# Performance work log

Measured on AMD Instinct MI355X. Metric: run time of the kernel, lower is better.

## Reference

```python
import jax, jax.numpy as jnp
import numpy as np
from jax import lax

EPS = 1e-5
DN = ('NCHW', 'OIHW', 'NCHW')

def _quant_global(w):
    scale = 1.0 / jnp.maximum(jnp.mean(jnp.abs(w)), EPS)
    u = jnp.clip(jnp.round(w * scale), -1.0, 1.0)
    return u, scale

def _quant_per_channel_dw(w):
    # w: [O, 1, kH, kW]; mean |w| over the kernel taps per output channel
    m = jnp.mean(jnp.abs(w).reshape(w.shape[0], w.shape[1], -1), axis=2, keepdims=True)
    scale = 1.0 / jnp.maximum(m, EPS)[..., None]          # [O,1,1,1]
    u = jnp.clip(jnp.round(w * scale), -1.0, 1.0)
    scale_bcast = jnp.transpose(scale, (1, 0, 2, 3))      # [1,O,1,1] broadcasts over y's channels
    return u, scale_bcast

def _ste(w_real, u):
    # straight-through estimator: forward uses u, grad flows to w_real
    return w_real + lax.stop_gradient(u - w_real)

def setup_inputs() -> dict:
    key = jax.random.key(0)
    k1, k2, k3 = jax.random.split(key, 3)
    x = jax.random.normal(k1, (16, 384, 56, 56), dtype=jnp.float32)
    w_dw = jax.random.normal(k2, (384, 1, 3, 3), dtype=jnp.float32) * 0.1
    w_pw = jax.random.normal(k3, (384, 384, 1, 1), dtype=jnp.float32) * 0.05
    return {"x": x, "w_dw": w_dw, "w_pw": w_pw}

def reference(x, w_dw, w_pw):
    C = x.shape[1]
    # depthwise HardTernaryConv (groups=in_chn, per-channel quant, pad=k//2)
    u_dw, s_dw = _quant_per_channel_dw(w_dw)
    y = lax.conv_general_dilated(x, _ste(w_dw, u_dw), window_strides=(1, 1),
                                 padding=((1, 1), (1, 1)),
                                 dimension_numbers=DN, feature_group_count=C)
    y = y / s_dw
    # pointwise 1x1 HardTernaryConv (global scalar quant scale)
    u_pw, s_pw = _quant_global(w_pw)
    y = lax.conv_general_dilated(y, _ste(w_pw, u_pw), window_strides=(1, 1),
                                 padding=((0, 0), (0, 0)), dimension_numbers=DN)
    y = y / s_pw
    return y
```

## Files before the change

### kernel.cpp

```cpp
#include <hip/hip_runtime.h>
#include <hip/hip_bf16.h>

#define CH 384
#define HH 56
#define WW 56
#define HW (HH*WW)
#define NN 16
#define BN 112
#define BK 64

#define XR_STRIDE 3840
#define YS_PITCH 18

typedef __attribute__((ext_vector_type(4))) float f32x4;
typedef __attribute__((ext_vector_type(8))) short bf16x8;
typedef __attribute__((ext_vector_type(4))) unsigned int u32x4;

__device__ float          g_wdw_eff[CH * 9];
__device__ __hip_bfloat16 g_wpw_u[CH * CH];
__device__ float          g_mx_pw;

__global__ __launch_bounds__(256) void partial_kernel(const float* __restrict__ wpw,
                                                      double* __restrict__ part) {
    const int t = threadIdx.x;
    const int base = blockIdx.x * 1536;
    double s = 0.0;
    #pragma unroll
    for (int k = 0; k < 6; ++k) s += (double)fabsf(wpw[base + t + k * 256]);
    #pragma unroll
    for (int off = 32; off > 0; off >>= 1) s += __shfl_down(s, off, 64);
    __shared__ double sred[4];
    if ((t & 63) == 0) sred[t >> 6] = s;
    __syncthreads();
    if (t == 0) part[blockIdx.x] = ((sred[0] + sred[1]) + sred[2]) + sred[3];
}

__global__ __launch_bounds__(512) void quant_kernel(const float* __restrict__ wdw,
                                                    const float* __restrict__ wpw,
                                                    const double* __restrict__ part) {
    const int t = threadIdx.x;
    __shared__ double pl[96];
    __shared__ float s_scale, s_mx;
    if (t < 96) pl[t] = part[t];
    __syncthreads();
    if (t == 0) {
        double tot = 0.0;
        #pragma unroll
        for (int i = 0; i < 96; ++i) tot += pl[i];
        const float mean = (float)(tot / (double)(CH * CH));
        const float mx   = fmaxf(mean, 1e-5f);
        s_mx = mx;
        s_scale = 1.0f / mx;
    }
    __syncthreads();
    const float scale = s_scale;

    const int base = blockIdx.x * 4096 + t * 8;
    const float4 a = *reinterpret_cast<const float4*>(wpw + base);
    const float4 b = *reinterpret_cast<const float4*>(wpw + base + 4);
    const float vin[8] = {a.x, a.y, a.z, a.w, b.x, b.y, b.z, b.w};
    bf16x8 uo;
    #pragma unroll
    for (int k = 0; k < 8; ++k) {
        float u = rintf(vin[k] * scale);
        u = fminf(1.f, fmaxf(-1.f, u));
        __hip_bfloat16 h = __float2bfloat16(u);
        uo[k] = *reinterpret_cast<short*>(&h);
    }
    *reinterpret_cast<bf16x8*>(g_wpw_u + base) = uo;

    if (blockIdx.x == 0) {
        if (t == 0) g_mx_pw = s_mx;
        if (t < CH) {
            const float* w = wdw + t * 9;
            float asum = 0.f;
            #pragma unroll
            for (int k = 0; k < 9; ++k) asum += fabsf(w[k]);
            const float mxd = fmaxf(asum / 9.0f, 1e-5f);
            const float scd = 1.0f / mxd;
            #pragma unroll
            for (int k = 0; k < 9; ++k) {
                float u = rintf(w[k] * scd);
                u = fminf(1.f, fmaxf(-1.f, u));
                g_wdw_eff[t * 9 + k] = u * mxd;
            }
        }
    }
}

__global__ __launch_bounds__(448, 4) void dw_kernel(const float* __restrict__ x,
                                                    __hip_bfloat16* __restrict__ y) {
    __shared__ __attribute__((aligned(16))) char xs[12 * XR_STRIDE];
    __shared__ __attribute__((aligned(16))) __hip_bfloat16 ys[224 * YS_PITCH];

    const int bid  = blockIdx.x;
    const int orig = (bid & 7) * 96 + (bid >> 3);
    const int nc   = orig >> 1;
    const int half = orig & 1;
    const int n    = nc / 24;
    const int cig  = nc % 24;
    const int ci0  = cig * 16;

    const int t    = threadIdx.x;
    const int wv   = t >> 6;
    const int lane = t & 63;

    const int cil = t & 15;
    const int rw  = t >> 4;
    const int row = rw / 7;
    const int wc  = rw % 7;
    const int w0  = wc * 8;

    const float* xg = x + ((size_t)n * CH + ci0) * HW;

    float wt[9];
    {
        const float* wdp = g_wdw_eff + (ci0 + cil) * 9;
        #pragma unroll
        for (int k = 0; k < 9; ++k) wt[k] = wdp[k];
    }

    const int hbase = half * 28;

    #pragma unroll
    for (int kk = 0; kk < 4; ++kk) {
        const int q = wv + 7 * kk;
        if (q < 24) {
            const int ro  = q >> 2;
            const int sub = q & 3;
            const int R   = hbase - 1 + ro;
            const int rr  = (R + 12) % 12;
            const int Rc  = R < 0 ? 0 : (R > HH - 1 ? HH - 1 : R);
            const int s   = sub * 64 + lane;
            const int sci = s / 15;
            const int scl = s - sci * 15;
            if (s < 240 && scl < 14) {
                __builtin_amdgcn_global_load_lds(
                    (const __attribute__((address_space(1))) void*)
                        (xg + (size_t)sci * HW + Rc * WW + scl * 4),
                    (__attribute__((address_space(3))) void*)
                        (xs + rr * XR_STRIDE + sub * 1024),
                    16, 0, 0);
            }
        }
    }

    #pragma unroll
    for (int i = 0; i < 7; ++i) {
        const int h0 = hbase + i * 4;

        if (i < 6) {
            const int RB = h0 + 5;
            #pragma unroll
            for (int kk = 0; kk < 3; ++kk) {
                const int q = wv + 7 * kk;
                if (q < 16) {
                    const int ro  = q >> 2;
                    const int sub = q & 3;
                    const int R   = RB + ro;
                    const int rr  = R % 12;
                    const int Rc  = R > HH - 1 ? HH - 1 : R;
                    const int s   = sub * 64 + lane;
                    const int sci = s / 15;
                    const int scl = s - sci * 15;
                    if (s < 240 && scl < 14) {
                        __builtin_amdgcn_global_load_lds(
                            (const __attribute__((address_space(1))) void*)
                                (xg + (size_t)sci * HW + Rc * WW + scl * 4),
                            (__attribute__((address_space(3))) void*)
                                (xs + rr * XR_STRIDE + sub * 1024),
                            16, 0, 0);
                    }
                }
            }
            if (wv < 2) asm volatile("s_waitcnt vmcnt(3)" ::: "memory");
            else        asm volatile("s_waitcnt vmcnt(2)" ::: "memory");
        } else {
            asm volatile("s_waitcnt vmcnt(0)" ::: "memory");
        }
        __builtin_amdgcn_s_barrier();
        __builtin_amdgcn_sched_barrier(0);

        const int h   = h0 + row;
        const int rrb = (h0 + 11) % 12;

        float acc[8] = {0.f, 0.f, 0.f, 0.f, 0.f, 0.f, 0.f, 0.f};
        #pragma unroll
        for (int r = 0; r < 3; ++r) {
            int rr = rrb + row + r; if (rr >= 12) rr -= 12;
            const char* rowp = xs + rr * XR_STRIDE + (cil * 15 + 2 * wc) * 16;
            const f32x4 f0 = *reinterpret_cast<const f32x4*>(rowp);
            const f32x4 f1 = *reinterpret_cast<const f32x4*>(rowp + 16);
            const float e0 = (wc > 0) ? *reinterpret_cast<const float*>(rowp - 4) : 0.f;
            const float f8 = *reinterpret_cast<const float*>(rowp + 32);
            const float x9 = (wc < 6) ? f8 : 0.f;
            const float xv[10] = {e0, f0.x, f0.y, f0.z, f0.w,
                                  f1.x, f1.y, f1.z, f1.w, x9};
            const bool dead = (r == 0 && h == 0) || (r == 2 && h == HH - 1);
            #pragma unroll
            for (int d = 0; d < 3; ++d) {
                const float w3 = dead ? 0.f : wt[r * 3 + d];
                #pragma unroll
                for (int j = 0; j < 8; ++j) acc[j] += w3 * xv[j + d];
            }
        }

        const int pxb = row * WW + w0;
        #pragma unroll
        for (int j = 0; j < 8; ++j)
            ys[(pxb + j) * YS_PITCH + cil] = __float2bfloat16(acc[j]);

        asm volatile("s_waitcnt lgkmcnt(0)" ::: "memory");
        __builtin_amdgcn_s_barrier();
        __builtin_amdgcn_sched_barrier(0);

        {
            const int px  = t >> 1;
            const int oct = t & 1;
            const unsigned* yp =
                reinterpret_cast<const unsigned*>(ys + px * YS_PITCH + oct * 8);
            u32x4 v;
            v.x = yp[0]; v.y = yp[1]; v.z = yp[2]; v.w = yp[3];
            *reinterpret_cast<u32x4*>(
                y + ((size_t)n * HW + (size_t)h0 * WW + px) * CH + ci0 + oct * 8) = v;
        }
        __builtin_amdgcn_sched_barrier(0);
    }
}

#define STAGE(B, KC) do {                                                         \
    const int _k0 = (KC) * BK;                                                    \
    _Pragma("unroll")                                                             \
    for (int _i = 0; _i < 4; ++_i) {                                              \
        const int _sb = wv * 4 + _i;                                              \
        if (_sb < 14) {                                                           \
            const int _s  = _sb * 64 + lane;                                      \
            const int _p  = _s >> 3;                                              \
            const int _c8 = (_s & 7) ^ (_p & 7);                                  \
            __builtin_amdgcn_global_load_lds(                                     \
                (const __attribute__((address_space(1))) void*)                  \
                    (yb + (size_t)_p * CH + _k0 + _c8 * 8),                       \
                (__attribute__((address_space(3))) void*)                        \
                    (&blds[(B)][0] + _sb * 512),                                  \
                16, 0, 0);                                                        \
        }                                                                         \
    }                                                                             \
} while (0)

#define LOADA(dst, KC) {                                                          \
    dst[0][0] = *reinterpret_cast<const bf16x8*>(ap0 + (KC) * 64);                \
    dst[0][1] = *reinterpret_cast<const bf16x8*>(ap0 + (KC) * 64 + 32);           \
    dst[1][0] = *reinterpret_cast<const bf16x8*>(ap1 + (KC) * 64);                \
    dst[1][1] = *reinterpret_cast<const bf16x8*>(ap1 + (KC) * 64 + 32); }

__global__ __launch_bounds__(256) void pw_kernel(const __hip_bfloat16* __restrict__ y,
                                                 float* __restrict__ out) {
    __shared__ __attribute__((aligned(16))) __hip_bfloat16 blds[2][BN * BK];

    const int bid  = blockIdx.x;
    const int orig = (bid & 7) * 168 + (bid >> 3);
    const int n  = orig / 84;
    const int r  = orig % 84;
    const int pt = r / 3;
    const int cb = r % 3;
    const int wv   = threadIdx.x >> 6;
    const int lane = threadIdx.x & 63;
    const int lr   = lane & 15;
    const int lk   = lane >> 4;

    const __hip_bfloat16* yb = y + ((size_t)n * HW + (size_t)pt * BN) * CH;
    const __hip_bfloat16* ap0 = g_wpw_u + (size_t)(cb * 128 + wv * 32 + lr) * CH + 8 * lk;
    const __hip_bfloat16* ap1 = ap0 + (size_t)16 * CH;

    f32x4 acc[2][7];
    #pragma unroll
    for (int i = 0; i < 2; ++i)
        #pragma unroll
        for (int j = 0; j < 7; ++j) acc[i][j] = (f32x4){0.f, 0.f, 0.f, 0.f};

    bf16x8 areg[2][2][2];
    STAGE(0, 0);
    LOADA(areg[0], 0);
    __syncthreads();

    #pragma unroll
    for (int kc = 0; kc < 6; ++kc) {
        const int cur = kc & 1;
        if (kc < 5) { STAGE(cur ^ 1, kc + 1); LOADA(areg[cur ^ 1], kc + 1); }
        #pragma unroll
        for (int kk = 0; kk < 2; ++kk) {
            bf16x8 bfr[7];
            #pragma unroll
            for (int j = 0; j < 7; ++j) {
                const int p  = 16 * j + lr;
                const int c8 = (kk * 4 + lk) ^ (p & 7);
                bfr[j] = *reinterpret_cast<const bf16x8*>(&blds[cur][p * 64 + c8 * 8]);
            }
            #pragma unroll
            for (int i = 0; i < 2; ++i)
                #pragma unroll
                for (int j = 0; j < 7; ++j)
                    acc[i][j] = __builtin_amdgcn_mfma_f32_16x16x32_bf16(
                        areg[cur][i][kk], bfr[j], acc[i][j], 0, 0, 0);
        }
        __syncthreads();
    }

    const float s = g_mx_pw;
    float* ob = out + (size_t)n * CH * HW + (size_t)pt * BN;
    #pragma unroll
    for (int i = 0; i < 2; ++i) {
        const int co0 = cb * 128 + wv * 32 + i * 16 + lk * 4;
        #pragma unroll
        for (int j = 0; j < 7; ++j) {
            const int px = 16 * j + lr;
            #pragma unroll
            for (int rr = 0; rr < 4; ++rr)
                ob[(size_t)(co0 + rr) * HW + px] = acc[i][j][rr] * s;
        }
    }
}

__global__ __launch_bounds__(512) void fused_kernel(const float* __restrict__ x,
                                                    float* __restrict__ out) {
    __shared__ __attribute__((aligned(16))) __hip_bfloat16 ylds[64 * CH];
    const int bid  = blockIdx.x;
    const int orig = (bid & 7) * 112 + (bid >> 3);
    const int n = orig / HH, h = orig % HH;
    const float* xn = x + (size_t)n * CH * HW;

    for (int u = threadIdx.x; u < CH * 7; u += 512) {
        const int ci = u / 7;
        const int wc = u % 7;
        const int w0 = wc * 8;
        const float* xp = xn + (size_t)ci * HW;
        const float* wd = g_wdw_eff + ci * 9;
        float acc[8] = {0.f, 0.f, 0.f, 0.f, 0.f, 0.f, 0.f, 0.f};
        #pragma unroll
        for (int dy = -1; dy <= 1; ++dy) {
            const int hh = h + dy;
            if (hh < 0 || hh >= HH) continue;
            const float* row = xp + hh * WW;
            const float4 va = *reinterpret_cast<const float4*>(row + w0);
            const float4 vb = *reinterpret_cast<const float4*>(row + w0 + 4);
            const float left  = (w0 > 0)      ? row[w0 - 1] : 0.f;
            const float right = (w0 + 8 < WW) ? row[w0 + 8] : 0.f;
            const float xv[10] = {left, va.x, va.y, va.z, va.w,
                                  vb.x, vb.y, vb.z, vb.w, right};
            #pragma unroll
            for (int dx = 0; dx < 3; ++dx) {
                const float wvv = wd[(dy + 1) * 3 + dx];
                #pragma unroll
                for (int j = 0; j < 8; ++j) acc[j] += xv[j + dx] * wvv;
            }
        }
        #pragma unroll
        for (int j = 0; j < 8; ++j)
            ylds[(w0 + j) * CH + (ci ^ ((j ^ wc) << 3))] = __float2bfloat16(acc[j]);
    }
    __syncthreads();

    const int wv   = threadIdx.x >> 6;
    const int lane = threadIdx.x & 63;
    const int lr   = lane & 15;
    const int lk   = lane >> 4;
    f32x4 acc[3][4];
    #pragma unroll
    for (int i = 0; i < 3; ++i)
        #pragma unroll
        for (int j = 0; j < 4; ++j) acc[i][j] = (f32x4){0.f, 0.f, 0.f, 0.f};
    const __hip_bfloat16* abase = g_wpw_u + (size_t)(wv * 16 + lr) * CH + 8 * lk;
    for (int k0 = 0; k0 < CH; k0 += 32) {
        bf16x8 bfr[4];
        #pragma unroll
        for (int j = 0; j < 4; ++j) {
            const int row = 16 * j + lr;
            const int sw  = ((row & 7) ^ ((row >> 3) & 7)) << 3;
            bfr[j] = *reinterpret_cast<const bf16x8*>(&ylds[row * CH + ((k0 + 8 * lk) ^ sw)]);
        }
        #pragma unroll
        for (int i = 0; i < 3; ++i) {
            const bf16x8 afr = *reinterpret_cast<const bf16x8*>(abase + (size_t)(i * 128) * CH + k0);
            #pragma unroll
            for (int j = 0; j < 4; ++j)
                acc[i][j] = __builtin_amdgcn_mfma_f32_16x16x32_bf16(afr, bfr[j], acc[i][j], 0, 0, 0);
        }
    }
    const float s = g_mx_pw;
    float* obase = out + (size_t)n * CH * HW + (size_t)h * WW;
    #pragma unroll
    for (int j = 0; j < 4; ++j) {
        const int pix = 16 * j + lr;
        if (pix >= WW) continue;
        #pragma unroll
        for (int i = 0; i < 3; ++i) {
            const int co0 = (wv + 8 * i) * 16 + lk * 4;
            #pragma unroll
            for (int rr = 0; rr < 4; ++rr)
                obase[(size_t)(co0 + rr) * HW + pix] = acc[i][j][rr] * s;
        }
    }
}

extern "C" void kernel_launch(void* const* d_in, const int* in_sizes, int n_in,
                              void* d_out, int out_size, void* d_ws, size_t ws_size,
                              hipStream_t stream) {
    const float* x    = (const float*)d_in[0];
    const float* w_dw = (const float*)d_in[1];
    const float* w_pw = (const float*)d_in[2];
    float* out = (float*)d_out;

    const size_t y_bytes    = (size_t)NN * HW * CH * sizeof(__hip_bfloat16);
    const size_t part_bytes = 96 * sizeof(double);

    if (ws_size >= y_bytes + part_bytes) {
        double* part = (double*)((char*)d_ws + y_bytes);
        partial_kernel<<<96, 256, 0, stream>>>(w_pw, part);
        quant_kernel<<<36, 512, 0, stream>>>(w_dw, w_pw, part);
        __hip_bfloat16* yg = (__hip_bfloat16*)d_ws;
        dw_kernel<<<768, 448, 0, stream>>>(x, yg);
        pw_kernel<<<NN * 28 * 3, 256, 0, stream>>>(yg, out);
    } else if (ws_size >= part_bytes) {
        double* part = (double*)d_ws;
        partial_kernel<<<96, 256, 0, stream>>>(w_pw, part);
        quant_kernel<<<36, 512, 0, stream>>>(w_dw, w_pw, part);
        fused_kernel<<<NN * HH, 512, 0, stream>>>(x, out);
    }
}
```

Before: 65.02 us.

## Retile depthwise kernel to 32 channels by quarter-height with smaller LDS ring

The depthwise stage now has each block cover 32 channels over a 14-row quarter of the image, processing 2 rows per step, where it used to cover 16 channels over half the image at 4 rows per step. The LDS row ring drops from 12 to 6 rows and the transposed bf16 staging buffer shrinks, so occupancy is raised to 6 blocks per CU. Output stores write 64 contiguous bytes of channels per pixel instead of 32. In exchange, halo rows are reloaded more often relative to useful rows, and the waitcnt schedule is more intricate.

```diff
diff --git a/kernel.cpp b/kernel.cpp
--- a/kernel.cpp
+++ b/kernel.cpp
@@ -9,8 +9,9 @@
 #define BN 112
 #define BK 64
 
-#define XR_STRIDE 3840
-#define YS_PITCH 18
+#define XRING 6
+#define XRROW 7168
+#define YSP 34
 
 typedef __attribute__((ext_vector_type(4))) float f32x4;
 typedef __attribute__((ext_vector_type(8))) short bf16x8;
@@ -88,30 +89,41 @@
     }
 }
 
-__global__ __launch_bounds__(448, 4) void dw_kernel(const float* __restrict__ x,
+__global__ __launch_bounds__(448, 6) void dw_kernel(const float* __restrict__ x,
                                                     __hip_bfloat16* __restrict__ y) {
-    __shared__ __attribute__((aligned(16))) char xs[12 * XR_STRIDE];
-    __shared__ __attribute__((aligned(16))) __hip_bfloat16 ys[224 * YS_PITCH];
+    __shared__ __attribute__((aligned(16))) char xs[XRING * XRROW];
+    __shared__ __attribute__((aligned(16))) __hip_bfloat16 ys[112 * YSP];
 
     const int bid  = blockIdx.x;
     const int orig = (bid & 7) * 96 + (bid >> 3);
-    const int nc   = orig >> 1;
-    const int half = orig & 1;
-    const int n    = nc / 24;
-    const int cig  = nc % 24;
-    const int ci0  = cig * 16;
+    const int n    = orig / 48;
+    const int rem  = orig - n * 48;
+    const int cig  = rem >> 2;
+    const int qtr  = rem & 3;
+    const int ci0  = cig * 32;
+    const int qb   = qtr * 14;
 
     const int t    = threadIdx.x;
     const int wv   = t >> 6;
     const int lane = t & 63;
 
-    const int cil = t & 15;
-    const int rw  = t >> 4;
-    const int row = rw / 7;
-    const int wc  = rw % 7;
-    const int w0  = wc * 8;
-
-    const float* xg = x + ((size_t)n * CH + ci0) * HW;
+    const int slot = wv * 64 + lane;
+    const int sci  = slot / 14;
+    const int scl  = slot - sci * 14;
+    const float* xg    = x + ((size_t)n * CH + ci0) * HW;
+    const float* sbase = xg + (size_t)sci * HW + scl * 4;
+    char* sdst = xs + wv * 1024;
+
+    const int cil  = t / 14;
+    const int rm   = t - cil * 14;
+    const int rowp = rm / 7;
+    const int wc   = rm - rowp * 7;
+    const int w0   = wc * 8;
+
+    const int dpx = t >> 2;
+    const int dg  = t & 3;
+    const int drow = (dpx >= WW) ? 1 : 0;
+    const int dw_  = dpx - drow * WW;
 
     float wt[9];
     {
@@ -120,80 +132,48 @@
         for (int k = 0; k < 9; ++k) wt[k] = wdp[k];
     }
 
-    const int hbase = half * 28;
-
-    #pragma unroll
-    for (int kk = 0; kk < 4; ++kk) {
-        const int q = wv + 7 * kk;
-        if (q < 24) {
-            const int ro  = q >> 2;
-            const int sub = q & 3;
-            const int R   = hbase - 1 + ro;
-            const int rr  = (R + 12) % 12;
-            const int Rc  = R < 0 ? 0 : (R > HH - 1 ? HH - 1 : R);
-            const int s   = sub * 64 + lane;
-            const int sci = s / 15;
-            const int scl = s - sci * 15;
-            if (s < 240 && scl < 14) {
+    #pragma unroll
+    for (int k = 0; k < 4; ++k) {
+        int R = qb - 1 + k;
+        const int rr = (R + XRING) % XRING;
+        R = R < 0 ? 0 : R;
+        __builtin_amdgcn_global_load_lds(
+            (const __attribute__((address_space(1))) void*)(sbase + (size_t)R * WW),
+            (__attribute__((address_space(3))) void*)(sdst + rr * XRROW), 16, 0, 0);
+    }
+
+    #pragma unroll
+    for (int i = 0; i < 7; ++i) {
+        const int h0 = qb + 2 * i;
+        if (i < 6) {
+            #pragma unroll
+            for (int k = 0; k < 2; ++k) {
+                int R = h0 + 3 + k;
+                const int rr = R % XRING;
+                R = R > HH - 1 ? HH - 1 : R;
                 __builtin_amdgcn_global_load_lds(
-                    (const __attribute__((address_space(1))) void*)
-                        (xg + (size_t)sci * HW + Rc * WW + scl * 4),
-                    (__attribute__((address_space(3))) void*)
-                        (xs + rr * XR_STRIDE + sub * 1024),
-                    16, 0, 0);
+                    (const __attribute__((address_space(1))) void*)(sbase + (size_t)R * WW),
+                    (__attribute__((address_space(3))) void*)(sdst + rr * XRROW), 16, 0, 0);
             }
-        }
-    }
-
-    #pragma unroll
-    for (int i = 0; i < 7; ++i) {
-        const int h0 = hbase + i * 4;
-
-        if (i < 6) {
-            const int RB = h0 + 5;
-            #pragma unroll
-            for (int kk = 0; kk < 3; ++kk) {
-                const int q = wv + 7 * kk;
-                if (q < 16) {
-                    const int ro  = q >> 2;
-                    const int sub = q & 3;
-                    const int R   = RB + ro;
-                    const int rr  = R % 12;
-                    const int Rc  = R > HH - 1 ? HH - 1 : R;
-                    const int s   = sub * 64 + lane;
-                    const int sci = s / 15;
-                    const int scl = s - sci * 15;
-                    if (s < 240 && scl < 14) {
-                        __builtin_amdgcn_global_load_lds(
-                            (const __attribute__((address_space(1))) void*)
-                                (xg + (size_t)sci * HW + Rc * WW + scl * 4),
-                            (__attribute__((address_space(3))) void*)
-                                (xs + rr * XR_STRIDE + sub * 1024),
-                            16, 0, 0);
-                    }
-                }
-            }
-            if (wv < 2) asm volatile("s_waitcnt vmcnt(3)" ::: "memory");
-            else        asm volatile("s_waitcnt vmcnt(2)" ::: "memory");
+            if (i == 0) asm volatile("s_waitcnt vmcnt(2)" ::: "memory");
+            else        asm volatile("s_waitcnt vmcnt(3)" ::: "memory");
         } else {
-            asm volatile("s_waitcnt vmcnt(0)" ::: "memory");
+            asm volatile("s_waitcnt vmcnt(1)" ::: "memory");
         }
         __builtin_amdgcn_s_barrier();
         __builtin_amdgcn_sched_barrier(0);
 
-        const int h   = h0 + row;
-        const int rrb = (h0 + 11) % 12;
-
+        const int h = h0 + rowp;
         float acc[8] = {0.f, 0.f, 0.f, 0.f, 0.f, 0.f, 0.f, 0.f};
         #pragma unroll
         for (int r = 0; r < 3; ++r) {
-            int rr = rrb + row + r; if (rr >= 12) rr -= 12;
-            const char* rowp = xs + rr * XR_STRIDE + (cil * 15 + 2 * wc) * 16;
-            const f32x4 f0 = *reinterpret_cast<const f32x4*>(rowp);
-            const f32x4 f1 = *reinterpret_cast<const f32x4*>(rowp + 16);
-            const float e0 = (wc > 0) ? *reinterpret_cast<const float*>(rowp - 4) : 0.f;
-            const float f8 = *reinterpret_cast<const float*>(rowp + 32);
-            const float x9 = (wc < 6) ? f8 : 0.f;
+            const int rr = (h - 1 + r + XRING) % XRING;
+            const char* rp = xs + rr * XRROW + cil * 224 + wc * 32;
+            const f32x4 f0 = *reinterpret_cast<const f32x4*>(rp);
+            const f32x4 f1 = *reinterpret_cast<const f32x4*>(rp + 16);
+            float e0 = 0.f, x9 = 0.f;
+            if (wc > 0) e0 = *reinterpret_cast<const float*>(rp - 4);
+            if (wc < 6) x9 = *reinterpret_cast<const float*>(rp + 32);
             const float xv[10] = {e0, f0.x, f0.y, f0.z, f0.w,
                                   f1.x, f1.y, f1.z, f1.w, x9};
             const bool dead = (r == 0 && h == 0) || (r == 2 && h == HH - 1);
@@ -204,25 +184,22 @@
                 for (int j = 0; j < 8; ++j) acc[j] += w3 * xv[j + d];
             }
         }
-
-        const int pxb = row * WW + w0;
         #pragma unroll
         for (int j = 0; j < 8; ++j)
-            ys[(pxb + j) * YS_PITCH + cil] = __float2bfloat16(acc[j]);
+            ys[(rowp * WW + w0 + j) * YSP + cil] = __float2bfloat16(acc[j]);
 
         asm volatile("s_waitcnt lgkmcnt(0)" ::: "memory");
         __builtin_amdgcn_s_barrier();
         __builtin_amdgcn_sched_barrier(0);
 
         {
-            const int px  = t >> 1;
-            const int oct = t & 1;
             const unsigned* yp =
-                reinterpret_cast<const unsigned*>(ys + px * YS_PITCH + oct * 8);
+                reinterpret_cast<const unsigned*>(ys + dpx * YSP + dg * 8);
             u32x4 v;
             v.x = yp[0]; v.y = yp[1]; v.z = yp[2]; v.w = yp[3];
             *reinterpret_cast<u32x4*>(
-                y + ((size_t)n * HW + (size_t)h0 * WW + px) * CH + ci0 + oct * 8) = v;
+                y + ((size_t)n * HW + (size_t)(h0 + drow) * WW + dw_) * CH
+                  + ci0 + dg * 8) = v;
         }
         __builtin_amdgcn_sched_barrier(0);
     }
```

Measured after the change: 68.42 us. 1.05x slower.
